# Optimization experiments

Hardware: AMD Instinct MI355X
Metric: run time of the kernel (lower is better)

The kernel has to match this reference:

```python
import jax, jax.numpy as jnp
import numpy as np

BATCH, N_BLOCKS, DC, N_QUBITS = 256, 32, 2, 12
DIM = 2 ** N_QUBITS


def setup_inputs() -> dict:
    key = jax.random.key(0)
    k1, k2, k3 = jax.random.split(key, 3)
    state_re = jax.random.normal(k1, (BATCH, N_BLOCKS, DC, DIM, 1), dtype=jnp.float32)
    state_im = jax.random.normal(k2, (BATCH, N_BLOCKS, DC, DIM, 1), dtype=jnp.float32)
    # nn.init.uniform_(weights, -pi/2, pi/2)
    weights = jax.random.uniform(k3, (1, N_BLOCKS, 1, N_QUBITS, 1), dtype=jnp.float32,
                                 minval=-np.pi / 2, maxval=np.pi / 2)
    return {"state_re": state_re, "state_im": state_im, "weights": weights}


def reference(state_re, state_im, weights):
    # Rz per qubit: diag(exp(-i w/2), exp(+i w/2)).
    # krons over qubits (qubit 0 most significant) yields a diagonal of length 2**Q:
    #   U[idx] = exp(-i/2 * sum_q w_q * s_q),  s_q = +1 if bit_q(idx)==0 else -1.
    n_qubits = weights.shape[3]
    dim = 2 ** n_qubits
    idx = jnp.arange(dim)
    bits = (idx[:, None] >> (n_qubits - 1 - jnp.arange(n_qubits))) & 1  # (dim, Q)
    signs = (1 - 2 * bits).astype(weights.dtype)                        # (dim, Q)
    w = weights[0, :, 0, :, 0]                                          # (n_blocks, Q)
    phase = jnp.einsum('bq,dq->bd', w, signs)                           # (n_blocks, dim)
    U = jnp.exp((-0.5j) * phase.astype(jnp.complex64))                  # diagonal kron product
    state = state_re + 1j * state_im                                    # (B, nb, dc, dim, 1)
    out = U[None, :, None, :, None] * state
    return jnp.stack([out.real, out.imag], axis=0)
```

## Files before the change

### kernel.cpp

```cpp
#include <hip/hip_runtime.h>

#define NQ     12
#define DIM    4096
#define TOTAL  67108864
#define N4     16777216

typedef float v4f __attribute__((ext_vector_type(4)));

__global__ __launch_bounds__(256) void rz_fused_kernel(
        const v4f* __restrict__ re, const v4f* __restrict__ im,
        const float* __restrict__ w,
        v4f* __restrict__ outr, v4f* __restrict__ outi) {
    int i = blockIdx.x * blockDim.x + threadIdx.x;
    if (i >= N4) return;
    int r  = i >> 10;
    int k  = (r >> 1) & 31;
    int d4 = i & 1023;
    int d0 = d4 << 2;

    const float* wk = w + k * NQ;
    float h = 0.f;
#pragma unroll
    for (int q = 0; q < 10; ++q) {
        float wq = wk[q];
        h += ((d0 >> (NQ - 1 - q)) & 1) ? -wq : wq;
    }
    float w10 = wk[10], w11 = wk[11];
    float c0, s0, c1, s1, c2, s2, c3, s3;
    __sincosf(0.5f * (h + w10 + w11), &s0, &c0);
    __sincosf(0.5f * (h + w10 - w11), &s1, &c1);
    __sincosf(0.5f * (h - w10 + w11), &s2, &c2);
    __sincosf(0.5f * (h - w10 - w11), &s3, &c3);

    v4f a = __builtin_nontemporal_load(re + i);
    v4f b = __builtin_nontemporal_load(im + i);
    v4f orv, oiv;
    orv.x = c0 * a.x + s0 * b.x;  oiv.x = c0 * b.x - s0 * a.x;
    orv.y = c1 * a.y + s1 * b.y;  oiv.y = c1 * b.y - s1 * a.y;
    orv.z = c2 * a.z + s2 * b.z;  oiv.z = c2 * b.z - s2 * a.z;
    orv.w = c3 * a.w + s3 * b.w;  oiv.w = c3 * b.w - s3 * a.w;
    __builtin_nontemporal_store(orv, outr + i);
    __builtin_nontemporal_store(oiv, outi + i);
}

extern "C" void kernel_launch(void* const* d_in, const int* in_sizes, int n_in,
                              void* d_out, int out_size, void* d_ws, size_t ws_size,
                              hipStream_t stream) {
    const v4f* re = (const v4f*)d_in[0];
    const v4f* im = (const v4f*)d_in[1];
    const float* w = (const float*)d_in[2];
    v4f* outr = (v4f*)d_out;
    v4f* outi = outr + N4;

    const int threads = 256;
    rz_fused_kernel<<<N4 / threads, threads, 0, stream>>>(re, im, w, outr, outi);
}
```

Baseline: 807.5 us.

## Precompute per-block phase cos/sin table in a separate kernel

Splits the work into two kernels. The first builds a 1 MB table of cos/sin values for each (block, dim) pair in workspace, and the streaming kernel reads from that table instead of recomputing the phase sum and four sincos per thread. The aim is to cut ALU work in the memory-bound streaming pass. In exchange it adds a second launch and a table read (32 bytes per thread) that should hit in cache.

Result: no change. 812.1 us (+0.6%).

```diff
diff --git a/kernel.cpp b/kernel.cpp
--- a/kernel.cpp
+++ b/kernel.cpp
@@ -2,22 +2,19 @@
 
 #define NQ     12
 #define DIM    4096
+#define NB     32
 #define TOTAL  67108864
 #define N4     16777216
+#define TAB4   32768
 
 typedef float v4f __attribute__((ext_vector_type(4)));
 
-__global__ __launch_bounds__(256) void rz_fused_kernel(
-        const v4f* __restrict__ re, const v4f* __restrict__ im,
-        const float* __restrict__ w,
-        v4f* __restrict__ outr, v4f* __restrict__ outi) {
-    int i = blockIdx.x * blockDim.x + threadIdx.x;
-    if (i >= N4) return;
-    int r  = i >> 10;
-    int k  = (r >> 1) & 31;
-    int d4 = i & 1023;
+__global__ __launch_bounds__(256) void rz_table_kernel(
+        const float* __restrict__ w, v4f* __restrict__ tab) {
+    int t = blockIdx.x * blockDim.x + threadIdx.x;
+    int k  = t >> 10;
+    int d4 = t & 1023;
     int d0 = d4 << 2;
-
     const float* wk = w + k * NQ;
     float h = 0.f;
 #pragma unroll
@@ -31,14 +28,31 @@
     __sincosf(0.5f * (h + w10 - w11), &s1, &c1);
     __sincosf(0.5f * (h - w10 + w11), &s2, &c2);
     __sincosf(0.5f * (h - w10 - w11), &s3, &c3);
+    v4f cs01, cs23;
+    cs01.x = c0; cs01.y = s0; cs01.z = c1; cs01.w = s1;
+    cs23.x = c2; cs23.y = s2; cs23.z = c3; cs23.w = s3;
+    tab[2 * t]     = cs01;
+    tab[2 * t + 1] = cs23;
+}
 
+__global__ __launch_bounds__(256) void rz_stream_kernel(
+        const v4f* __restrict__ re, const v4f* __restrict__ im,
+        const v4f* __restrict__ tab,
+        v4f* __restrict__ outr, v4f* __restrict__ outi) {
+    int i = blockIdx.x * blockDim.x + threadIdx.x;
+    int r  = i >> 10;
+    int k  = (r >> 1) & 31;
+    int d4 = i & 1023;
+    int t  = (k << 10) | d4;
+    v4f cs01 = tab[2 * t];
+    v4f cs23 = tab[2 * t + 1];
     v4f a = __builtin_nontemporal_load(re + i);
     v4f b = __builtin_nontemporal_load(im + i);
     v4f orv, oiv;
-    orv.x = c0 * a.x + s0 * b.x;  oiv.x = c0 * b.x - s0 * a.x;
-    orv.y = c1 * a.y + s1 * b.y;  oiv.y = c1 * b.y - s1 * a.y;
-    orv.z = c2 * a.z + s2 * b.z;  oiv.z = c2 * b.z - s2 * a.z;
-    orv.w = c3 * a.w + s3 * b.w;  oiv.w = c3 * b.w - s3 * a.w;
+    orv.x = cs01.x * a.x + cs01.y * b.x;  oiv.x = cs01.x * b.x - cs01.y * a.x;
+    orv.y = cs01.z * a.y + cs01.w * b.y;  oiv.y = cs01.z * b.y - cs01.w * a.y;
+    orv.z = cs23.x * a.z + cs23.y * b.z;  oiv.z = cs23.x * b.z - cs23.y * a.z;
+    orv.w = cs23.z * a.w + cs23.w * b.w;  oiv.w = cs23.z * b.w - cs23.w * a.w;
     __builtin_nontemporal_store(orv, outr + i);
     __builtin_nontemporal_store(oiv, outi + i);
 }
@@ -51,7 +65,8 @@
     const float* w = (const float*)d_in[2];
     v4f* outr = (v4f*)d_out;
     v4f* outi = outr + N4;
+    v4f* tab  = (v4f*)d_ws;
 
-    const int threads = 256;
-    rz_fused_kernel<<<N4 / threads, threads, 0, stream>>>(re, im, w, outr, outi);
+    rz_table_kernel<<<TAB4 / 256, 256, 0, stream>>>(w, tab);
+    rz_stream_kernel<<<N4 / 256, 256, 0, stream>>>(re, im, tab, outr, outi);
 }
```
